# Optimization experiments

Measured on AMD Instinct MI355X. Metric: run time of the kernel, lower is better.

The kernel has to match this reference:

```python
import jax, jax.numpy as jnp
import numpy as np

N, E, B, EP = 100000, 1600000, 512, 200000
NIN, NEMB, HID, NL = 64, 64, 72, 3
EPS = 1e-5


def setup_inputs() -> dict:
    key = jax.random.key(0)
    ks = jax.random.split(key, 20)
    inp = {
        'x': jax.random.normal(ks[0], (N, NIN), jnp.float32),
        'emb': jax.random.normal(ks[1], (N, NEMB), jnp.float32),
        'assign': jax.random.uniform(ks[2], (N, B), jnp.float32),
        'edge_index': jax.random.randint(ks[3], (2, E), 0, N, jnp.int64),
        'pedge_index': jax.random.randint(ks[4], (2, EP), 0, B, jnp.int64),
        # params (xavier-ish scale)
        'node_w': jax.random.normal(ks[5], (NIN, HID), jnp.float32) / np.sqrt(NIN),
        'node_b': jnp.zeros((HID,), jnp.float32),
        'emb_w': jax.random.normal(ks[6], (NEMB, HID), jnp.float32) / np.sqrt(NEMB),
        'emb_b': jnp.zeros((HID,), jnp.float32),
        'conv_winit': jax.random.normal(ks[7], (NL, HID, HID), jnp.float32) / np.sqrt(HID),
        'conv_wroot': jax.random.normal(ks[8], (NL, HID, HID), jnp.float32) / np.sqrt(HID),
        'conv_bias': jnp.zeros((NL, HID), jnp.float32),
        'bn_gamma': jnp.ones((NL, HID), jnp.float32),
        'bn_beta': jnp.zeros((NL, HID), jnp.float32),
        'mlp_w1': jax.random.normal(ks[9], (12 * HID, HID), jnp.float32) / np.sqrt(12 * HID),
        'mlp_b1': jnp.zeros((HID,), jnp.float32),
        'mlp_w2': jax.random.normal(ks[10], (HID, 1), jnp.float32) / np.sqrt(HID),
        'mlp_b2': jnp.zeros((1,), jnp.float32),
    }
    return inp


def _forward(x, emb, assign, node_w, node_b, emb_w, emb_b, conv_winit,
             conv_wroot, conv_bias, bn_gamma, bn_beta, mlp_w1, mlp_b1,
             mlp_w2, mlp_b2, edge_index, pedge_index):
    n = x.shape[0]
    nb = assign.shape[1]
    row, col = edge_index[0], edge_index[1]
    # gcn_norm without self-loops (ARMAConv): D^{-1/2} A D^{-1/2}
    deg = jax.ops.segment_sum(jnp.ones((row.shape[0],), x.dtype), col, num_segments=n)
    dis = jnp.where(deg > 0, jax.lax.rsqrt(jnp.maximum(deg, 1.0)) * jnp.where(deg > 0, 1.0, 0.0), 0.0)
    dis = jnp.where(deg > 0, deg ** -0.5, 0.0)
    norm = dis[row] * dis[col]

    h = jax.nn.relu(x @ node_w + node_b)  # [N, HID]
    for l in range(NL):
        # ARMAConv K=1, T=1: relu(A_hat (h Wi) + h Wr + b)
        m = norm[:, None] * (h @ conv_winit[l])[row]        # [E, HID]
        agg = jax.ops.segment_sum(m, col, num_segments=n)   # [N, HID]
        h = jax.nn.relu(agg + h @ conv_wroot[l] + conv_bias[l])
        # F.relu applied again in forward (idempotent), then BatchNorm (training stats)
        mu = h.mean(0)
        var = ((h - mu) ** 2).mean(0)
        h = (h - mu) * jax.lax.rsqrt(var + EPS) * bn_gamma[l] + bn_beta[l]

    e = jax.nn.relu(emb @ emb_w + emb_b)
    z = jnp.concatenate([h, e], axis=-1)  # [N, 2*HID]

    batch = jnp.argmax(assign, axis=-1)
    cnt = jax.ops.segment_sum(jnp.ones((n,), z.dtype), batch, num_segments=nb)
    p1 = jax.ops.segment_sum(z, batch, num_segments=nb)
    p2 = jax.ops.segment_max(z, batch, num_segments=nb)
    p3 = p1 / jnp.maximum(cnt, 1.0)[:, None]
    xp = jnp.concatenate([p1, p2, p3], axis=-1)  # [B, 6*HID]

    pair = jnp.concatenate([xp[pedge_index[0]], xp[pedge_index[1]]], axis=1)  # [EP, 12*HID]
    out = jnp.tanh(pair @ mlp_w1 + mlp_b1) @ mlp_w2 + mlp_b2
    return out


def reference(x, emb, assign, edge_index, pedge_index, node_w, node_b, emb_w,
              emb_b, conv_winit, conv_wroot, conv_bias, bn_gamma, bn_beta,
              mlp_w1, mlp_b1, mlp_w2, mlp_b2):
    return _forward(x, emb, assign, node_w, node_b, emb_w, emb_b, conv_winit,
                    conv_wroot, conv_bias, bn_gamma, bn_beta, mlp_w1, mlp_b1,
                    mlp_w2, mlp_b2, edge_index, pedge_index)
```

## Files before the change

kernel.cpp:

```cpp
#include <hip/hip_runtime.h>
#include <hip/hip_bf16.h>

#define HID 72
#define EPSV 1e-5f
#define CAP 64
#define DP 76
#define GF 384
#define GA 2048

__device__ __forceinline__ float tanh_fast(float x) {
    float cx = fminf(fmaxf(x, -15.f), 15.f);
    float e = __expf(2.f * cx);
    return __fdividef(e - 1.f, e + 1.f);
}
__device__ __forceinline__ void fma4(float4& a, float w, const float4 v) {
    a.x += w * v.x; a.y += w * v.y; a.z += w * v.z; a.w += w * v.w;
}
__device__ __forceinline__ float inv_sqrt_deg(int d) {
    return (d > 0) ? rsqrtf((float)d) : 0.f;
}

__global__ __launch_bounds__(256) void k_d1(const float* __restrict__ x, const float* __restrict__ node_w,
                                            const float* __restrict__ node_b, float* __restrict__ t_buf,
                                            int* __restrict__ deg, float* __restrict__ stats,
                                            int* __restrict__ bcnt, int N, int B, int GD) {
    __shared__ float ws[HID][DP];
    int tid = threadIdx.x;
    int bid = blockIdx.x;
    if (bid >= GD) {
        int j = (bid - GD) * 256 + tid;
        if (j < N) deg[j] = 0;
        if (j < 3 * 2 * HID) stats[j] = 0.f;
        if (j < B) bcnt[j] = 0;
        return;
    }
    int n0 = bid * 128;
    for (int i = tid; i < 64 * HID; i += 256) {
        int k = i / HID, f = i % HID;
        ws[f][k] = node_w[i];
    }
    __syncthreads();
    int tn = tid & 31;
    int tf = (tid >> 5) * 9;
    float acc[4][9];
    #pragma unroll
    for (int j = 0; j < 9; j++) {
        float b = node_b[tf + j];
        acc[0][j] = b; acc[1][j] = b; acc[2][j] = b; acc[3][j] = b;
    }
    int g0 = n0 + tn;
    const float4* xp0 = (const float4*)(x + (size_t)(g0      < N ? g0      : N - 1) * 64);
    const float4* xp1 = (const float4*)(x + (size_t)(g0 + 32 < N ? g0 + 32 : N - 1) * 64);
    const float4* xp2 = (const float4*)(x + (size_t)(g0 + 64 < N ? g0 + 64 : N - 1) * 64);
    const float4* xp3 = (const float4*)(x + (size_t)(g0 + 96 < N ? g0 + 96 : N - 1) * 64);
    #pragma unroll 2
    for (int k4 = 0; k4 < 16; k4++) {
        float4 h0 = xp0[k4];
        float4 h1 = xp1[k4];
        float4 h2 = xp2[k4];
        float4 h3 = xp3[k4];
        int k = k4 * 4;
        #pragma unroll
        for (int j = 0; j < 9; j++) {
            float4 w = *(const float4*)&ws[tf + j][k];
            acc[0][j] += h0.x * w.x + h0.y * w.y + h0.z * w.z + h0.w * w.w;
            acc[1][j] += h1.x * w.x + h1.y * w.y + h1.z * w.z + h1.w * w.w;
            acc[2][j] += h2.x * w.x + h2.y * w.y + h2.z * w.z + h2.w * w.w;
            acc[3][j] += h3.x * w.x + h3.y * w.y + h3.z * w.z + h3.w * w.w;
        }
    }
    #pragma unroll
    for (int i = 0; i < 4; i++) {
        int gn = n0 + tn + 32 * i;
        if (gn >= N) continue;
        float* dst = t_buf + (size_t)gn * HID + tf;
        #pragma unroll
        for (int j = 0; j < 9; j++) dst[j] = fmaxf(acc[i][j], 0.f);
    }
}

__global__ __launch_bounds__(256) void k_front2(const int* __restrict__ row, const int* __restrict__ col,
                                                int* __restrict__ deg, int* __restrict__ csr_r, int E,
                                                const float* __restrict__ wi0, const float* __restrict__ wr0,
                                                const float* __restrict__ cb0, float* __restrict__ t_buf,
                                                float* __restrict__ hw,
                                                const float* __restrict__ emb, const float* __restrict__ emb_w,
                                                const float* __restrict__ emb_b, float* __restrict__ e_buf,
                                                const float* __restrict__ assign, int* __restrict__ batchv,
                                                int* __restrict__ bcnt, int N, int B, int GDE, int GC) {
    __shared__ float ws2[2 * HID][DP];
    int tid = threadIdx.x;
    int bid = blockIdx.x;

    if (bid < GF) {
        int stride = GF * 256 * 8;
        for (int base = (bid * 256 + tid) * 8; base < E; base += stride) {
            #pragma unroll
            for (int h = 0; h < 2; h++) {
                int eb = base + h * 4;
                if (eb + 3 < E) {
                    int4 cc = *(const int4*)(col + eb);
                    int4 rr = *(const int4*)(row + eb);
                    int p0 = atomicAdd(&deg[cc.x], 1);
                    int p1 = atomicAdd(&deg[cc.y], 1);
                    int p2 = atomicAdd(&deg[cc.z], 1);
                    int p3 = atomicAdd(&deg[cc.w], 1);
                    if (p0 < CAP) csr_r[(size_t)cc.x * CAP + p0] = rr.x;
                    if (p1 < CAP) csr_r[(size_t)cc.y * CAP + p1] = rr.y;
                    if (p2 < CAP) csr_r[(size_t)cc.z * CAP + p2] = rr.z;
                    if (p3 < CAP) csr_r[(size_t)cc.w * CAP + p3] = rr.w;
                } else if (eb < E) {
                    int lim = (eb + 4 < E) ? eb + 4 : E;
                    for (int e = eb; e < lim; e++) {
                        int c = col[e];
                        int pos = atomicAdd(&deg[c], 1);
                        if (pos < CAP) csr_r[(size_t)c * CAP + pos] = row[e];
                    }
                }
            }
        }
        return;
    }
    bid -= GF;
    if (bid < GC) {
        int n0 = bid * 64;
        for (int i = tid; i < HID * 2 * HID; i += 256) {
            int k = i / (2 * HID), f = i % (2 * HID);
            ws2[f][k] = (f < HID) ? wi0[k * HID + f] : wr0[k * HID + (f - HID)];
        }
        __syncthreads();
        int tn = tid & 15;
        int tf = (tid >> 4) * 9;
        float acc[4][9];
        #pragma unroll
        for (int j = 0; j < 9; j++) {
            float b = (tf >= HID) ? cb0[tf - HID + j] : 0.f;
            acc[0][j] = b; acc[1][j] = b; acc[2][j] = b; acc[3][j] = b;
        }
        int g0 = n0 + tn;
        const float* r0 = t_buf + (size_t)(g0      < N ? g0      : N - 1) * HID;
        const float* r1 = t_buf + (size_t)(g0 + 16 < N ? g0 + 16 : N - 1) * HID;
        const float* r2 = t_buf + (size_t)(g0 + 32 < N ? g0 + 32 : N - 1) * HID;
        const float* r3 = t_buf + (size_t)(g0 + 48 < N ? g0 + 48 : N - 1) * HID;
        #pragma unroll 2
        for (int k4 = 0; k4 < HID / 4; k4++) {
            int k = k4 * 4;
            float4 h0 = *(const float4*)(r0 + k);
            float4 h1 = *(const float4*)(r1 + k);
            float4 h2 = *(const float4*)(r2 + k);
            float4 h3 = *(const float4*)(r3 + k);
            #pragma unroll
            for (int j = 0; j < 9; j++) {
                float4 w = *(const float4*)&ws2[tf + j][k];
                acc[0][j] += h0.x * w.x + h0.y * w.y + h0.z * w.z + h0.w * w.w;
                acc[1][j] += h1.x * w.x + h1.y * w.y + h1.z * w.z + h1.w * w.w;
                acc[2][j] += h2.x * w.x + h2.y * w.y + h2.z * w.z + h2.w * w.w;
                acc[3][j] += h3.x * w.x + h3.y * w.y + h3.z * w.z + h3.w * w.w;
            }
        }
        __syncthreads();
        #pragma unroll
        for (int i = 0; i < 4; i++) {
            int gn = n0 + tn + 16 * i;
            if (gn >= N) continue;
            float* dst = (tf < HID) ? (hw + (size_t)gn * HID + tf) : (t_buf + (size_t)gn * HID + (tf - HID));
            #pragma unroll
            for (int j = 0; j < 9; j++) dst[j] = acc[i][j];
        }
        return;
    }
    bid -= GC;
    if (bid < GDE) {
        int n0 = bid * 128;
        for (int i = tid; i < 64 * HID; i += 256) {
            int k = i / HID, f = i % HID;
            ws2[f][k] = emb_w[i];
        }
        __syncthreads();
        int tn = tid & 31;
        int tf = (tid >> 5) * 9;
        float acc[4][9];
        #pragma unroll
        for (int j = 0; j < 9; j++) {
            float b = emb_b[tf + j];
            acc[0][j] = b; acc[1][j] = b; acc[2][j] = b; acc[3][j] = b;
        }
        int g0 = n0 + tn;
        const float4* xp0 = (const float4*)(emb + (size_t)(g0      < N ? g0      : N - 1) * 64);
        const float4* xp1 = (const float4*)(emb + (size_t)(g0 + 32 < N ? g0 + 32 : N - 1) * 64);
        const float4* xp2 = (const float4*)(emb + (size_t)(g0 + 64 < N ? g0 + 64 : N - 1) * 64);
        const float4* xp3 = (const float4*)(emb + (size_t)(g0 + 96 < N ? g0 + 96 : N - 1) * 64);
        #pragma unroll 2
        for (int k4 = 0; k4 < 16; k4++) {
            float4 h0 = xp0[k4];
            float4 h1 = xp1[k4];
            float4 h2 = xp2[k4];
            float4 h3 = xp3[k4];
            int k = k4 * 4;
            #pragma unroll
            for (int j = 0; j < 9; j++) {
                float4 w = *(const float4*)&ws2[tf + j][k];
                acc[0][j] += h0.x * w.x + h0.y * w.y + h0.z * w.z + h0.w * w.w;
                acc[1][j] += h1.x * w.x + h1.y * w.y + h1.z * w.z + h1.w * w.w;
                acc[2][j] += h2.x * w.x + h2.y * w.y + h2.z * w.z + h2.w * w.w;
                acc[3][j] += h3.x * w.x + h3.y * w.y + h3.z * w.z + h3.w * w.w;
            }
        }
        #pragma unroll
        for (int i = 0; i < 4; i++) {
            int gn = n0 + tn + 32 * i;
            if (gn >= N) continue;
            float* dst = e_buf + (size_t)gn * HID + tf;
            #pragma unroll
            for (int j = 0; j < 9; j++) dst[j] = fmaxf(acc[i][j], 0.f);
        }
        return;
    }
    bid -= GDE;
    int wib = tid >> 6;
    int lane = tid & 63;
    int nq = B / 4;
    for (int n = bid * 4 + wib; n < N; n += GA * 4) {
        const float4* rp4 = (const float4*)(assign + (size_t)n * B);
        float best = -INFINITY;
        int bidx = 0x7fffffff;
        for (int q = lane; q < nq; q += 64) {
            float4 v = rp4[q];
            int j = q * 4;
            if (v.x > best) { best = v.x; bidx = j; }
            if (v.y > best) { best = v.y; bidx = j + 1; }
            if (v.z > best) { best = v.z; bidx = j + 2; }
            if (v.w > best) { best = v.w; bidx = j + 3; }
        }
        #pragma unroll
        for (int off = 32; off > 0; off >>= 1) {
            float ov = __shfl_down(best, off);
            int oi = __shfl_down(bidx, off);
            if (ov > best || (ov == best && oi < bidx)) { best = ov; bidx = oi; }
        }
        if (lane == 0) {
            batchv[n] = bidx;
            atomicAdd(&bcnt[bidx], 1);
        }
    }
}

__global__ __launch_bounds__(256) void k_gather9(const float* __restrict__ hw, const int* __restrict__ deg,
                                                 const int* __restrict__ csr_r, float* t, int N,
                                                 int scanB, const int* __restrict__ bcnt,
                                                 int* __restrict__ boffs, int* __restrict__ bcur) {
    if (scanB && blockIdx.x == gridDim.x - 1) {
        int lane = threadIdx.x;
        if (lane < 64) {
            int c[8];
            int tot = 0;
            int base = lane * 8;
            #pragma unroll
            for (int j = 0; j < 8; j++) {
                int idx = base + j;
                c[j] = (idx < scanB) ? bcnt[idx] : 0;
                tot += c[j];
            }
            int v = tot;
            #pragma unroll
            for (int off = 1; off < 64; off <<= 1) {
                int u = __shfl_up(v, off);
                if (lane >= off) v += u;
            }
            int run = v - tot;
            #pragma unroll
            for (int j = 0; j < 8; j++) {
                int idx = base + j;
                if (idx < scanB) {
                    boffs[idx] = run;
                    bcur[idx] = run;
                    run += c[j];
                }
            }
        }
        return;
    }
    int tid = blockIdx.x * blockDim.x + threadIdx.x;
    int n = tid / 9;
    int s = tid - n * 9;
    if (n >= N) return;
    float4* trow = (float4*)(t + (size_t)n * HID) + s * 2;
    float4 a0 = trow[0], a1 = trow[1];
    int dn = deg[n];
    int d = (dn > CAP) ? CAP : dn;
    float disc = inv_sqrt_deg(dn);
    const int* crow = csr_r + (size_t)n * CAP;
    const float4* hb = (const float4*)hw + s * 2;
    for (int j0 = 0; j0 < d; j0 += 4) {
        int4 rr = *(const int4*)(crow + j0);
        int rem = d - j0;
        {
            float w = disc * inv_sqrt_deg(deg[rr.x]);
            const float4* hp = hb + (size_t)rr.x * 18;
            fma4(a0, w, hp[0]); fma4(a1, w, hp[1]);
        }
        if (rem > 1) {
            float w = disc * inv_sqrt_deg(deg[rr.y]);
            const float4* hp = hb + (size_t)rr.y * 18;
            fma4(a0, w, hp[0]); fma4(a1, w, hp[1]);
        }
        if (rem > 2) {
            float w = disc * inv_sqrt_deg(deg[rr.z]);
            const float4* hp = hb + (size_t)rr.z * 18;
            fma4(a0, w, hp[0]); fma4(a1, w, hp[1]);
        }
        if (rem > 3) {
            float w = disc * inv_sqrt_deg(deg[rr.w]);
            const float4* hp = hb + (size_t)rr.w * 18;
            fma4(a0, w, hp[0]); fma4(a1, w, hp[1]);
        }
    }
    trow[0] = make_float4(fmaxf(a0.x, 0.f), fmaxf(a0.y, 0.f), fmaxf(a0.z, 0.f), fmaxf(a0.w, 0.f));
    trow[1] = make_float4(fmaxf(a1.x, 0.f), fmaxf(a1.y, 0.f), fmaxf(a1.z, 0.f), fmaxf(a1.w, 0.f));
}

#define CP 76
__global__ __launch_bounds__(256) void k_conv_t(const float* t, const float* __restrict__ stats,
                                                const float* __restrict__ gamma, const float* __restrict__ beta,
                                                const float* __restrict__ wi, const float* __restrict__ wr,
                                                const float* __restrict__ cb, float* __restrict__ hw,
                                                float* agg, int N, float invN, int gcBlocks,
                                                const int* __restrict__ batchv, int* __restrict__ bcur,
                                                int* __restrict__ nlist) {
    __shared__ float hs[64][CP];
    __shared__ float ws[2 * HID][CP];
    int tid = threadIdx.x;
    if ((int)blockIdx.x >= gcBlocks) {
        int n = ((int)blockIdx.x - gcBlocks) * 256 + tid;
        if (n < N) {
            int b = batchv[n];
            int pos = atomicAdd(&bcur[b], 1);
            nlist[pos] = n;
        }
        return;
    }
    int n0 = blockIdx.x * 64;
    for (int i = tid; i < HID * 2 * HID; i += 256) {
        int k = i / (2 * HID), f = i % (2 * HID);
        ws[f][k] = (f < HID) ? wi[k * HID + f] : wr[k * HID + (f - HID)];
    }
    for (int i = tid; i < 64 * HID; i += 256) {
        int n = i / HID, f = i % HID;
        int gn = n0 + n;
        float v = (gn < N) ? t[(size_t)gn * HID + f] : 0.f;
        float mu = stats[f] * invN;
        float var = stats[HID + f] * invN - mu * mu;
        v = (v - mu) * rsqrtf(var + EPSV) * gamma[f] + beta[f];
        hs[n][f] = v;
    }
    __syncthreads();
    int tn = tid & 15;
    int tf = (tid >> 4) * 9;
    float acc[4][9];
    #pragma unroll
    for (int j = 0; j < 9; j++) {
        float b = (tf >= HID) ? cb[tf - HID + j] : 0.f;
        acc[0][j] = b; acc[1][j] = b; acc[2][j] = b; acc[3][j] = b;
    }
    #pragma unroll 2
    for (int k4 = 0; k4 < HID / 4; k4++) {
        int k = k4 * 4;
        float4 h0 = *(const float4*)&hs[tn][k];
        float4 h1 = *(const float4*)&hs[tn + 16][k];
        float4 h2 = *(const float4*)&hs[tn + 32][k];
        float4 h3 = *(const float4*)&hs[tn + 48][k];
        #pragma unroll
        for (int j = 0; j < 9; j++) {
            float4 w = *(const float4*)&ws[tf + j][k];
            acc[0][j] += h0.x * w.x + h0.y * w.y + h0.z * w.z + h0.w * w.w;
            acc[1][j] += h1.x * w.x + h1.y * w.y + h1.z * w.z + h1.w * w.w;
            acc[2][j] += h2.x * w.x + h2.y * w.y + h2.z * w.z + h2.w * w.w;
            acc[3][j] += h3.x * w.x + h3.y * w.y + h3.z * w.z + h3.w * w.w;
        }
    }
    #pragma unroll
    for (int i = 0; i < 4; i++) {
        int gn = n0 + tn + 16 * i;
        if (gn >= N) continue;
        float* dst = (tf < HID) ? (hw + (size_t)gn * HID + tf) : (agg + (size_t)gn * HID + (tf - HID));
        #pragma unroll
        for (int j = 0; j < 9; j++) dst[j] = acc[i][j];
    }
}

__global__ __launch_bounds__(256) void k_stats(const float* __restrict__ t, float* __restrict__ st, int total4) {
    __shared__ float s1[HID], s2[HID];
    int tx = threadIdx.x;
    if (tx < HID) s1[tx] = 0.f;
    else if (tx < 2 * HID) s2[tx - HID] = 0.f;
    __syncthreads();
    int stride = gridDim.x * blockDim.x;
    int i0 = blockIdx.x * blockDim.x + tx;
    int f0 = (i0 * 4) % HID;
    float a0 = 0, a1 = 0, a2 = 0, a3 = 0, q0 = 0, q1 = 0, q2 = 0, q3 = 0;
    const float4* tp = (const float4*)t;
    for (int i = i0; i < total4; i += stride) {
        float4 v = tp[i];
        a0 += v.x; q0 += v.x * v.x;
        a1 += v.y; q1 += v.y * v.y;
        a2 += v.z; q2 += v.z * v.z;
        a3 += v.w; q3 += v.w * v.w;
    }
    atomicAdd(&s1[f0 + 0], a0); atomicAdd(&s2[f0 + 0], q0);
    atomicAdd(&s1[f0 + 1], a1); atomicAdd(&s2[f0 + 1], q1);
    atomicAdd(&s1[f0 + 2], a2); atomicAdd(&s2[f0 + 2], q2);
    atomicAdd(&s1[f0 + 3], a3); atomicAdd(&s2[f0 + 3], q3);
    __syncthreads();
    if (tx < HID) {
        atomicAdd(&st[tx], s1[tx]);
        atomicAdd(&st[HID + tx], s2[tx]);
    }
}

__global__ __launch_bounds__(576) void k_poolB(const float* __restrict__ t2, const float* __restrict__ ebuf,
                                               const float* __restrict__ stats2, const float* __restrict__ g2,
                                               const float* __restrict__ bt2, const int* __restrict__ boffs,
                                               const int* __restrict__ bcnt, const int* __restrict__ nlist,
                                               float* __restrict__ xp, float invN) {
    __shared__ float ls[4][2 * HID], lm[4][2 * HID];
    int b = blockIdx.x;
    int tid = threadIdx.x;
    int f = tid % (2 * HID);
    int ch = tid / (2 * HID);
    bool isH = f < HID;
    float a = 1.f, sh = 0.f;
    const float* src;
    if (isH) {
        float s1v = stats2[f], s2v = stats2[HID + f];
        float mu = s1v * invN;
        float var = s2v * invN - mu * mu;
        float inv = rsqrtf(var + EPSV);
        a = inv * g2[f];
        sh = bt2[f] - mu * a;
        src = t2 + f;
    } else {
        src = ebuf + (f - HID);
    }
    int s = boffs[b];
    int c = bcnt[b];
    int e = s + c;
    float sum = 0.f, mx = -INFINITY;
    for (int i = s + ch; i < e; i += 4) {
        float v = src[(size_t)nlist[i] * HID] * a + sh;
        sum += v;
        mx = fmaxf(mx, v);
    }
    ls[ch][f] = sum;
    lm[ch][f] = mx;
    __syncthreads();
    if (ch == 0) {
        float stot = ls[0][f] + ls[1][f] + ls[2][f] + ls[3][f];
        float mtot = fmaxf(fmaxf(lm[0][f], lm[1][f]), fmaxf(lm[2][f], lm[3][f]));
        float* xr = xp + (size_t)b * (6 * HID);
        xr[f] = stot;
        xr[2 * HID + f] = mtot;
        xr[4 * HID + f] = stot / fmaxf((float)c, 1.f);
    }
}

__global__ __launch_bounds__(192) void k_uv(const float* __restrict__ xp, const float* __restrict__ w1,
                                            const float* __restrict__ b1, float* __restrict__ U,
                                            float* __restrict__ V) {
    int b = blockIdx.x;
    int t = threadIdx.x;
    if (t >= 2 * HID) return;
    int half = t / HID;
    int f = t % HID;
    const float* xr = xp + (size_t)b * (6 * HID);
    const float* wb = w1 + (size_t)half * (6 * HID) * HID + f;
    float acc = (half == 0) ? b1[f] : 0.f;
    #pragma unroll 4
    for (int k = 0; k < 6 * HID; k++) acc += xr[k] * wb[(size_t)k * HID];
    if (half == 0) U[(size_t)b * HID + f] = acc;
    else           V[(size_t)b * HID + f] = acc;
}

__global__ __launch_bounds__(256) void k_edge(const int* __restrict__ pe, const float* __restrict__ U,
                                              const float* __restrict__ V, const float* __restrict__ w2,
                                              const float* __restrict__ b2, float* __restrict__ out, int EP) {
    int ep = blockIdx.x * blockDim.x + threadIdx.x;
    if (ep >= EP) return;
    int a = pe[ep];
    int b = pe[EP + ep];
    const float4* up = (const float4*)(U + (size_t)a * HID);
    const float4* vp = (const float4*)(V + (size_t)b * HID);
    float s = 0.f;
    #pragma unroll
    for (int q = 0; q < HID / 4; q++) {
        float4 u = up[q];
        float4 v = vp[q];
        s += tanh_fast(u.x + v.x) * w2[q * 4 + 0];
        s += tanh_fast(u.y + v.y) * w2[q * 4 + 1];
        s += tanh_fast(u.z + v.z) * w2[q * 4 + 2];
        s += tanh_fast(u.w + v.w) * w2[q * 4 + 3];
    }
    out[ep] = s + b2[0];
}

extern "C" void kernel_launch(void* const* d_in, const int* in_sizes, int n_in,
                              void* d_out, int out_size, void* d_ws, size_t ws_size,
                              hipStream_t stream) {
    const float* x       = (const float*)d_in[0];
    const float* emb     = (const float*)d_in[1];
    const float* assign  = (const float*)d_in[2];
    const int*   ei      = (const int*)d_in[3];
    const int*   pe      = (const int*)d_in[4];
    const float* node_w  = (const float*)d_in[5];
    const float* node_b  = (const float*)d_in[6];
    const float* emb_w   = (const float*)d_in[7];
    const float* emb_b   = (const float*)d_in[8];
    const float* conv_wi = (const float*)d_in[9];
    const float* conv_wr = (const float*)d_in[10];
    const float* conv_b  = (const float*)d_in[11];
    const float* bn_g    = (const float*)d_in[12];
    const float* bn_b    = (const float*)d_in[13];
    const float* w1      = (const float*)d_in[14];
    const float* b1      = (const float*)d_in[15];
    const float* w2      = (const float*)d_in[16];
    const float* b2      = (const float*)d_in[17];

    int N = in_sizes[0] / 64;
    int B = in_sizes[2] / N;
    int E = in_sizes[3] / 2;
    int EP = in_sizes[4] / 2;
    float invN = 1.0f / (float)N;

    char* wp = (char*)d_ws;
    auto alloc = [&](size_t nbytes) -> void* {
        void* p = (void*)wp;
        wp += (nbytes + 255) & ~(size_t)255;
        return p;
    };
    float* t_buf  = (float*)alloc((size_t)N * HID * 4);
    float* hw     = (float*)alloc((size_t)N * HID * 4);
    float* e_buf  = (float*)alloc((size_t)N * HID * 4);
    int*   csr_r  = (int*)alloc((size_t)N * CAP * 4);
    int*   deg    = (int*)alloc((size_t)N * 4);
    int*   batchv = (int*)alloc((size_t)N * 4);
    int*   nlist  = (int*)alloc((size_t)N * 4);
    float* stats  = (float*)alloc((size_t)3 * 2 * HID * 4);
    int*   bcnt   = (int*)alloc((size_t)B * 4);
    int*   boffs  = (int*)alloc((size_t)B * 4);
    int*   bcur   = (int*)alloc((size_t)B * 4);
    float* xp     = (float*)alloc((size_t)B * 6 * HID * 4);
    float* Ub     = (float*)alloc((size_t)B * HID * 4);
    float* Vb     = (float*)alloc((size_t)B * HID * 4);

    const int* row = ei;
    const int* col = ei + E;

    int GD = (N + 127) / 128;
    int GC = (N + 63) / 64;
    int GZ = (N + 255) / 256;
    int GG = (9 * N + 255) / 256;

    k_d1<<<GD + GZ, 256, 0, stream>>>(x, node_w, node_b, t_buf, deg, stats, bcnt, N, B, GD);

    k_front2<<<GF + GC + GD + GA, 256, 0, stream>>>(row, col, deg, csr_r, E,
                                                    conv_wi, conv_wr, conv_b, t_buf, hw,
                                                    emb, emb_w, emb_b, e_buf,
                                                    assign, batchv, bcnt, N, B, GD, GC);

    k_gather9<<<GG + 1, 256, 0, stream>>>(hw, deg, csr_r, t_buf, N, B, bcnt, boffs, bcur);
    k_stats<<<288, 256, 0, stream>>>(t_buf, stats, N * HID / 4);

    k_conv_t<<<GC + GZ, 256, 0, stream>>>(t_buf, stats, bn_g, bn_b,
                                          conv_wi + (size_t)HID * HID, conv_wr + (size_t)HID * HID,
                                          conv_b + HID, hw, t_buf, N, invN, GC, batchv, bcur, nlist);
    k_gather9<<<GG, 256, 0, stream>>>(hw, deg, csr_r, t_buf, N, 0, nullptr, nullptr, nullptr);
    k_stats<<<288, 256, 0, stream>>>(t_buf, stats + 2 * HID, N * HID / 4);

    k_conv_t<<<GC, 256, 0, stream>>>(t_buf, stats + 2 * HID, bn_g + HID, bn_b + HID,
                                     conv_wi + (size_t)2 * HID * HID, conv_wr + (size_t)2 * HID * HID,
                                     conv_b + 2 * HID, hw, t_buf, N, invN, GC, nullptr, nullptr, nullptr);
    k_gather9<<<GG, 256, 0, stream>>>(hw, deg, csr_r, t_buf, N, 0, nullptr, nullptr, nullptr);
    k_stats<<<288, 256, 0, stream>>>(t_buf, stats + 4 * HID, N * HID / 4);

    k_poolB<<<B, 576, 0, stream>>>(t_buf, e_buf, stats + 4 * HID,
                                   bn_g + 2 * HID, bn_b + 2 * HID,
                                   boffs, bcnt, nlist, xp, invN);
    k_uv<<<B, 192, 0, stream>>>(xp, w1, b1, Ub, Vb);
    k_edge<<<(EP + 255) / 256, 256, 0, stream>>>(pe, Ub, Vb, w2, b2, (float*)d_out, EP);
}
```

Baseline: 1.227 ms.

## Fuse BN stats into gather, prescale hw by source degree, rebalance front kernels

Removes the three k_stats passes by accumulating per-feature sum and sum of squares inside the gather kernel, using block-level shared atomics and then 32 shadow copies in global memory to spread contention. conv_t now multiplies hw by the source node's inverse sqrt degree, so later gathers add neighbour rows without looking up each neighbour's degree. The emb projection moves into k_d1, and the layer-0 conv is split into separate Wi and Wr blocks, with the root term written to a new t2 buffer instead of in place. The costs are an extra N×HID buffer, per-element shared atomics in the gather, and reduced-order float sums for the statistics.

Result: slower. 1.316 ms (+7.2%).

```diff
diff --git a/kernel.cpp b/kernel.cpp
--- a/kernel.cpp
+++ b/kernel.cpp
@@ -5,7 +5,8 @@
 #define EPSV 1e-5f
 #define CAP 64
 #define DP 76
-#define GF 384
+#define NSH 32
+#define GF 256
 #define GA 2048
 
 __device__ __forceinline__ float tanh_fast(float x) {
@@ -16,28 +17,37 @@
 __device__ __forceinline__ void fma4(float4& a, float w, const float4 v) {
     a.x += w * v.x; a.y += w * v.y; a.z += w * v.z; a.w += w * v.w;
 }
+__device__ __forceinline__ void add4(float4& a, const float4 v) {
+    a.x += v.x; a.y += v.y; a.z += v.z; a.w += v.w;
+}
 __device__ __forceinline__ float inv_sqrt_deg(int d) {
     return (d > 0) ? rsqrtf((float)d) : 0.f;
 }
 
 __global__ __launch_bounds__(256) void k_d1(const float* __restrict__ x, const float* __restrict__ node_w,
-                                            const float* __restrict__ node_b, float* __restrict__ t_buf,
-                                            int* __restrict__ deg, float* __restrict__ stats,
+                                            const float* __restrict__ node_b,
+                                            const float* __restrict__ emb, const float* __restrict__ emb_w,
+                                            const float* __restrict__ emb_b,
+                                            float* __restrict__ t_buf, float* __restrict__ e_buf,
+                                            int* __restrict__ deg, float* __restrict__ shadows,
                                             int* __restrict__ bcnt, int N, int B, int GD) {
     __shared__ float ws[HID][DP];
     int tid = threadIdx.x;
     int bid = blockIdx.x;
-    if (bid >= GD) {
-        int j = (bid - GD) * 256 + tid;
+    if (bid >= 2 * GD) {
+        int j = (bid - 2 * GD) * 256 + tid;
         if (j < N) deg[j] = 0;
-        if (j < 3 * 2 * HID) stats[j] = 0.f;
+        if (j < 3 * NSH * 2 * HID) shadows[j] = 0.f;
         if (j < B) bcnt[j] = 0;
         return;
     }
+    const float* xin; const float* W; const float* bias; float* out;
+    if (bid < GD) { xin = x;   W = node_w; bias = node_b; out = t_buf; }
+    else          { xin = emb; W = emb_w;  bias = emb_b;  out = e_buf; bid -= GD; }
     int n0 = bid * 128;
     for (int i = tid; i < 64 * HID; i += 256) {
         int k = i / HID, f = i % HID;
-        ws[f][k] = node_w[i];
+        ws[f][k] = W[i];
     }
     __syncthreads();
     int tn = tid & 31;
@@ -45,14 +55,14 @@
     float acc[4][9];
     #pragma unroll
     for (int j = 0; j < 9; j++) {
-        float b = node_b[tf + j];
+        float b = bias[tf + j];
         acc[0][j] = b; acc[1][j] = b; acc[2][j] = b; acc[3][j] = b;
     }
     int g0 = n0 + tn;
-    const float4* xp0 = (const float4*)(x + (size_t)(g0      < N ? g0      : N - 1) * 64);
-    const float4* xp1 = (const float4*)(x + (size_t)(g0 + 32 < N ? g0 + 32 : N - 1) * 64);
-    const float4* xp2 = (const float4*)(x + (size_t)(g0 + 64 < N ? g0 + 64 : N - 1) * 64);
-    const float4* xp3 = (const float4*)(x + (size_t)(g0 + 96 < N ? g0 + 96 : N - 1) * 64);
+    const float4* xp0 = (const float4*)(xin + (size_t)(g0      < N ? g0      : N - 1) * 64);
+    const float4* xp1 = (const float4*)(xin + (size_t)(g0 + 32 < N ? g0 + 32 : N - 1) * 64);
+    const float4* xp2 = (const float4*)(xin + (size_t)(g0 + 64 < N ? g0 + 64 : N - 1) * 64);
+    const float4* xp3 = (const float4*)(xin + (size_t)(g0 + 96 < N ? g0 + 96 : N - 1) * 64);
     #pragma unroll 2
     for (int k4 = 0; k4 < 16; k4++) {
         float4 h0 = xp0[k4];
@@ -73,7 +83,7 @@
     for (int i = 0; i < 4; i++) {
         int gn = n0 + tn + 32 * i;
         if (gn >= N) continue;
-        float* dst = t_buf + (size_t)gn * HID + tf;
+        float* dst = out + (size_t)gn * HID + tf;
         #pragma unroll
         for (int j = 0; j < 9; j++) dst[j] = fmaxf(acc[i][j], 0.f);
     }
@@ -81,14 +91,13 @@
 
 __global__ __launch_bounds__(256) void k_front2(const int* __restrict__ row, const int* __restrict__ col,
                                                 int* __restrict__ deg, int* __restrict__ csr_r, int E,
+                                                const float* __restrict__ t_buf,
                                                 const float* __restrict__ wi0, const float* __restrict__ wr0,
-                                                const float* __restrict__ cb0, float* __restrict__ t_buf,
-                                                float* __restrict__ hw,
-                                                const float* __restrict__ emb, const float* __restrict__ emb_w,
-                                                const float* __restrict__ emb_b, float* __restrict__ e_buf,
+                                                const float* __restrict__ cb0,
+                                                float* __restrict__ hw, float* __restrict__ t2,
                                                 const float* __restrict__ assign, int* __restrict__ batchv,
-                                                int* __restrict__ bcnt, int N, int B, int GDE, int GC) {
-    __shared__ float ws2[2 * HID][DP];
+                                                int* __restrict__ bcnt, int N, int B, int GC) {
+    __shared__ float ws[HID][DP];
     int tid = threadIdx.x;
     int bid = blockIdx.x;
 
@@ -122,26 +131,29 @@
         return;
     }
     bid -= GF;
-    if (bid < GC) {
-        int n0 = bid * 64;
-        for (int i = tid; i < HID * 2 * HID; i += 256) {
-            int k = i / (2 * HID), f = i % (2 * HID);
-            ws2[f][k] = (f < HID) ? wi0[k * HID + f] : wr0[k * HID + (f - HID)];
+    if (bid < 2 * GC) {
+        const float* W; const float* bias; float* out;
+        if (bid < GC) { W = wi0; bias = nullptr; out = hw; }
+        else          { W = wr0; bias = cb0;     out = t2; bid -= GC; }
+        int n0 = bid * 128;
+        for (int i = tid; i < HID * HID; i += 256) {
+            int k = i / HID, f = i % HID;
+            ws[f][k] = W[i];
         }
         __syncthreads();
-        int tn = tid & 15;
-        int tf = (tid >> 4) * 9;
+        int tn = tid & 31;
+        int tf = (tid >> 5) * 9;
         float acc[4][9];
         #pragma unroll
         for (int j = 0; j < 9; j++) {
-            float b = (tf >= HID) ? cb0[tf - HID + j] : 0.f;
+            float b = bias ? bias[tf + j] : 0.f;
             acc[0][j] = b; acc[1][j] = b; acc[2][j] = b; acc[3][j] = b;
         }
         int g0 = n0 + tn;
         const float* r0 = t_buf + (size_t)(g0      < N ? g0      : N - 1) * HID;
-        const float* r1 = t_buf + (size_t)(g0 + 16 < N ? g0 + 16 : N - 1) * HID;
-        const float* r2 = t_buf + (size_t)(g0 + 32 < N ? g0 + 32 : N - 1) * HID;
-        const float* r3 = t_buf + (size_t)(g0 + 48 < N ? g0 + 48 : N - 1) * HID;
+        const float* r1 = t_buf + (size_t)(g0 + 32 < N ? g0 + 32 : N - 1) * HID;
+        const float* r2 = t_buf + (size_t)(g0 + 64 < N ? g0 + 64 : N - 1) * HID;
+        const float* r3 = t_buf + (size_t)(g0 + 96 < N ? g0 + 96 : N - 1) * HID;
         #pragma unroll 2
         for (int k4 = 0; k4 < HID / 4; k4++) {
             int k = k4 * 4;
@@ -151,72 +163,24 @@
             float4 h3 = *(const float4*)(r3 + k);
             #pragma unroll
             for (int j = 0; j < 9; j++) {
-                float4 w = *(const float4*)&ws2[tf + j][k];
+                float4 w = *(const float4*)&ws[tf + j][k];
                 acc[0][j] += h0.x * w.x + h0.y * w.y + h0.z * w.z + h0.w * w.w;
                 acc[1][j] += h1.x * w.x + h1.y * w.y + h1.z * w.z + h1.w * w.w;
                 acc[2][j] += h2.x * w.x + h2.y * w.y + h2.z * w.z + h2.w * w.w;
                 acc[3][j] += h3.x * w.x + h3.y * w.y + h3.z * w.z + h3.w * w.w;
             }
         }
-        __syncthreads();
-        #pragma unroll
-        for (int i = 0; i < 4; i++) {
-            int gn = n0 + tn + 16 * i;
-            if (gn >= N) continue;
-            float* dst = (tf < HID) ? (hw + (size_t)gn * HID + tf) : (t_buf + (size_t)gn * HID + (tf - HID));
-            #pragma unroll
-            for (int j = 0; j < 9; j++) dst[j] = acc[i][j];
-        }
-        return;
-    }
-    bid -= GC;
-    if (bid < GDE) {
-        int n0 = bid * 128;
-        for (int i = tid; i < 64 * HID; i += 256) {
-            int k = i / HID, f = i % HID;
-            ws2[f][k] = emb_w[i];
-        }
-        __syncthreads();
-        int tn = tid & 31;
-        int tf = (tid >> 5) * 9;
-        float acc[4][9];
-        #pragma unroll
-        for (int j = 0; j < 9; j++) {
-            float b = emb_b[tf + j];
-            acc[0][j] = b; acc[1][j] = b; acc[2][j] = b; acc[3][j] = b;
-        }
-        int g0 = n0 + tn;
-        const float4* xp0 = (const float4*)(emb + (size_t)(g0      < N ? g0      : N - 1) * 64);
-        const float4* xp1 = (const float4*)(emb + (size_t)(g0 + 32 < N ? g0 + 32 : N - 1) * 64);
-        const float4* xp2 = (const float4*)(emb + (size_t)(g0 + 64 < N ? g0 + 64 : N - 1) * 64);
-        const float4* xp3 = (const float4*)(emb + (size_t)(g0 + 96 < N ? g0 + 96 : N - 1) * 64);
-        #pragma unroll 2
-        for (int k4 = 0; k4 < 16; k4++) {
-            float4 h0 = xp0[k4];
-            float4 h1 = xp1[k4];
-            float4 h2 = xp2[k4];
-            float4 h3 = xp3[k4];
-            int k = k4 * 4;
-            #pragma unroll
-            for (int j = 0; j < 9; j++) {
-                float4 w = *(const float4*)&ws2[tf + j][k];
-                acc[0][j] += h0.x * w.x + h0.y * w.y + h0.z * w.z + h0.w * w.w;
-                acc[1][j] += h1.x * w.x + h1.y * w.y + h1.z * w.z + h1.w * w.w;
-                acc[2][j] += h2.x * w.x + h2.y * w.y + h2.z * w.z + h2.w * w.w;
-                acc[3][j] += h3.x * w.x + h3.y * w.y + h3.z * w.z + h3.w * w.w;
-            }
-        }
         #pragma unroll
         for (int i = 0; i < 4; i++) {
             int gn = n0 + tn + 32 * i;
             if (gn >= N) continue;
-            float* dst = e_buf + (size_t)gn * HID + tf;
-            #pragma unroll
-            for (int j = 0; j < 9; j++) dst[j] = fmaxf(acc[i][j], 0.f);
+            float* dst = out + (size_t)gn * HID + tf;
+            #pragma unroll
+            for (int j = 0; j < 9; j++) dst[j] = acc[i][j];
         }
         return;
     }
-    bid -= GDE;
+    bid -= 2 * GC;
     int wib = tid >> 6;
     int lane = tid & 63;
     int nq = B / 4;
@@ -245,8 +209,10 @@
     }
 }
 
+template <int SCALED>
 __global__ __launch_bounds__(256) void k_gather9(const float* __restrict__ hw, const int* __restrict__ deg,
-                                                 const int* __restrict__ csr_r, float* t, int N,
+                                                 const int* __restrict__ csr_r, const float* __restrict__ t2,
+                                                 float* __restrict__ t, int N, float* __restrict__ shadow,
                                                  int scanB, const int* __restrict__ bcnt,
                                                  int* __restrict__ boffs, int* __restrict__ bcur) {
     if (scanB && blockIdx.x == gridDim.x - 1) {
@@ -280,55 +246,83 @@
         }
         return;
     }
-    int tid = blockIdx.x * blockDim.x + threadIdx.x;
+    __shared__ float s1[HID], s2[HID];
+    int tx = threadIdx.x;
+    if (tx < HID) { s1[tx] = 0.f; s2[tx] = 0.f; }
+    __syncthreads();
+    int tid = blockIdx.x * blockDim.x + tx;
     int n = tid / 9;
     int s = tid - n * 9;
-    if (n >= N) return;
-    float4* trow = (float4*)(t + (size_t)n * HID) + s * 2;
-    float4 a0 = trow[0], a1 = trow[1];
-    int dn = deg[n];
-    int d = (dn > CAP) ? CAP : dn;
-    float disc = inv_sqrt_deg(dn);
-    const int* crow = csr_r + (size_t)n * CAP;
-    const float4* hb = (const float4*)hw + s * 2;
-    for (int j0 = 0; j0 < d; j0 += 4) {
-        int4 rr = *(const int4*)(crow + j0);
-        int rem = d - j0;
-        {
-            float w = disc * inv_sqrt_deg(deg[rr.x]);
-            const float4* hp = hb + (size_t)rr.x * 18;
-            fma4(a0, w, hp[0]); fma4(a1, w, hp[1]);
-        }
-        if (rem > 1) {
-            float w = disc * inv_sqrt_deg(deg[rr.y]);
-            const float4* hp = hb + (size_t)rr.y * 18;
-            fma4(a0, w, hp[0]); fma4(a1, w, hp[1]);
-        }
-        if (rem > 2) {
-            float w = disc * inv_sqrt_deg(deg[rr.z]);
-            const float4* hp = hb + (size_t)rr.z * 18;
-            fma4(a0, w, hp[0]); fma4(a1, w, hp[1]);
-        }
-        if (rem > 3) {
-            float w = disc * inv_sqrt_deg(deg[rr.w]);
-            const float4* hp = hb + (size_t)rr.w * 18;
-            fma4(a0, w, hp[0]); fma4(a1, w, hp[1]);
-        }
-    }
-    trow[0] = make_float4(fmaxf(a0.x, 0.f), fmaxf(a0.y, 0.f), fmaxf(a0.z, 0.f), fmaxf(a0.w, 0.f));
-    trow[1] = make_float4(fmaxf(a1.x, 0.f), fmaxf(a1.y, 0.f), fmaxf(a1.z, 0.f), fmaxf(a1.w, 0.f));
+    if (n < N) {
+        const float4* t2row = (const float4*)(t2 + (size_t)n * HID) + s * 2;
+        float4 a0 = t2row[0], a1 = t2row[1];
+        float4 b0 = make_float4(0.f, 0.f, 0.f, 0.f), b1 = b0;
+        int dn = deg[n];
+        int d = (dn > CAP) ? CAP : dn;
+        float disc = inv_sqrt_deg(dn);
+        const int* crow = csr_r + (size_t)n * CAP;
+        const float4* hb = (const float4*)hw + s * 2;
+        for (int j0 = 0; j0 < d; j0 += 4) {
+            int4 rr = *(const int4*)(crow + j0);
+            int rem = d - j0;
+            {
+                const float4* hp = hb + (size_t)rr.x * 18;
+                if (SCALED) { add4(b0, hp[0]); add4(b1, hp[1]); }
+                else { float w = inv_sqrt_deg(deg[rr.x]); fma4(b0, w, hp[0]); fma4(b1, w, hp[1]); }
+            }
+            if (rem > 1) {
+                const float4* hp = hb + (size_t)rr.y * 18;
+                if (SCALED) { add4(b0, hp[0]); add4(b1, hp[1]); }
+                else { float w = inv_sqrt_deg(deg[rr.y]); fma4(b0, w, hp[0]); fma4(b1, w, hp[1]); }
+            }
+            if (rem > 2) {
+                const float4* hp = hb + (size_t)rr.z * 18;
+                if (SCALED) { add4(b0, hp[0]); add4(b1, hp[1]); }
+                else { float w = inv_sqrt_deg(deg[rr.z]); fma4(b0, w, hp[0]); fma4(b1, w, hp[1]); }
+            }
+            if (rem > 3) {
+                const float4* hp = hb + (size_t)rr.w * 18;
+                if (SCALED) { add4(b0, hp[0]); add4(b1, hp[1]); }
+                else { float w = inv_sqrt_deg(deg[rr.w]); fma4(b0, w, hp[0]); fma4(b1, w, hp[1]); }
+            }
+        }
+        fma4(a0, disc, b0);
+        fma4(a1, disc, b1);
+        a0 = make_float4(fmaxf(a0.x, 0.f), fmaxf(a0.y, 0.f), fmaxf(a0.z, 0.f), fmaxf(a0.w, 0.f));
+        a1 = make_float4(fmaxf(a1.x, 0.f), fmaxf(a1.y, 0.f), fmaxf(a1.z, 0.f), fmaxf(a1.w, 0.f));
+        float4* trow = (float4*)(t + (size_t)n * HID) + s * 2;
+        trow[0] = a0;
+        trow[1] = a1;
+        int f0 = s * 8;
+        atomicAdd(&s1[f0 + 0], a0.x); atomicAdd(&s2[f0 + 0], a0.x * a0.x);
+        atomicAdd(&s1[f0 + 1], a0.y); atomicAdd(&s2[f0 + 1], a0.y * a0.y);
+        atomicAdd(&s1[f0 + 2], a0.z); atomicAdd(&s2[f0 + 2], a0.z * a0.z);
+        atomicAdd(&s1[f0 + 3], a0.w); atomicAdd(&s2[f0 + 3], a0.w * a0.w);
+        atomicAdd(&s1[f0 + 4], a1.x); atomicAdd(&s2[f0 + 4], a1.x * a1.x);
+        atomicAdd(&s1[f0 + 5], a1.y); atomicAdd(&s2[f0 + 5], a1.y * a1.y);
+        atomicAdd(&s1[f0 + 6], a1.z); atomicAdd(&s2[f0 + 6], a1.z * a1.z);
+        atomicAdd(&s1[f0 + 7], a1.w); atomicAdd(&s2[f0 + 7], a1.w * a1.w);
+    }
+    __syncthreads();
+    if (tx < HID) {
+        float* shrow = shadow + (size_t)(blockIdx.x & (NSH - 1)) * (2 * HID);
+        atomicAdd(&shrow[tx], s1[tx]);
+        atomicAdd(&shrow[HID + tx], s2[tx]);
+    }
 }
 
 #define CP 76
-__global__ __launch_bounds__(256) void k_conv_t(const float* t, const float* __restrict__ stats,
+__global__ __launch_bounds__(256) void k_conv_t(const float* __restrict__ t, const float* __restrict__ shadow,
                                                 const float* __restrict__ gamma, const float* __restrict__ beta,
                                                 const float* __restrict__ wi, const float* __restrict__ wr,
                                                 const float* __restrict__ cb, float* __restrict__ hw,
-                                                float* agg, int N, float invN, int gcBlocks,
+                                                float* __restrict__ t2, const int* __restrict__ deg,
+                                                int N, float invN, int gcBlocks,
                                                 const int* __restrict__ batchv, int* __restrict__ bcur,
                                                 int* __restrict__ nlist) {
     __shared__ float hs[64][CP];
     __shared__ float ws[2 * HID][CP];
+    __shared__ float bns[2 * HID];
     int tid = threadIdx.x;
     if ((int)blockIdx.x >= gcBlocks) {
         int n = ((int)blockIdx.x - gcBlocks) * 256 + tid;
@@ -339,17 +333,24 @@
         }
         return;
     }
-    int n0 = blockIdx.x * 64;
+    if (tid < 2 * HID) {
+        float ssum = 0.f;
+        #pragma unroll
+        for (int c = 0; c < NSH; c++) ssum += shadow[c * 2 * HID + tid];
+        bns[tid] = ssum;
+    }
     for (int i = tid; i < HID * 2 * HID; i += 256) {
         int k = i / (2 * HID), f = i % (2 * HID);
         ws[f][k] = (f < HID) ? wi[k * HID + f] : wr[k * HID + (f - HID)];
     }
+    __syncthreads();
+    int n0 = blockIdx.x * 64;
     for (int i = tid; i < 64 * HID; i += 256) {
         int n = i / HID, f = i % HID;
         int gn = n0 + n;
         float v = (gn < N) ? t[(size_t)gn * HID + f] : 0.f;
-        float mu = stats[f] * invN;
-        float var = stats[HID + f] * invN - mu * mu;
+        float mu = bns[f] * invN;
+        float var = bns[HID + f] * invN - mu * mu;
         v = (v - mu) * rsqrtf(var + EPSV) * gamma[f] + beta[f];
         hs[n][f] = v;
     }
@@ -382,43 +383,21 @@
     for (int i = 0; i < 4; i++) {
         int gn = n0 + tn + 16 * i;
         if (gn >= N) continue;
-        float* dst = (tf < HID) ? (hw + (size_t)gn * HID + tf) : (agg + (size_t)gn * HID + (tf - HID));
-        #pragma unroll
-        for (int j = 0; j < 9; j++) dst[j] = acc[i][j];
-    }
-}
-
-__global__ __launch_bounds__(256) void k_stats(const float* __restrict__ t, float* __restrict__ st, int total4) {
-    __shared__ float s1[HID], s2[HID];
-    int tx = threadIdx.x;
-    if (tx < HID) s1[tx] = 0.f;
-    else if (tx < 2 * HID) s2[tx - HID] = 0.f;
-    __syncthreads();
-    int stride = gridDim.x * blockDim.x;
-    int i0 = blockIdx.x * blockDim.x + tx;
-    int f0 = (i0 * 4) % HID;
-    float a0 = 0, a1 = 0, a2 = 0, a3 = 0, q0 = 0, q1 = 0, q2 = 0, q3 = 0;
-    const float4* tp = (const float4*)t;
-    for (int i = i0; i < total4; i += stride) {
-        float4 v = tp[i];
-        a0 += v.x; q0 += v.x * v.x;
-        a1 += v.y; q1 += v.y * v.y;
-        a2 += v.z; q2 += v.z * v.z;
-        a3 += v.w; q3 += v.w * v.w;
-    }
-    atomicAdd(&s1[f0 + 0], a0); atomicAdd(&s2[f0 + 0], q0);
-    atomicAdd(&s1[f0 + 1], a1); atomicAdd(&s2[f0 + 1], q1);
-    atomicAdd(&s1[f0 + 2], a2); atomicAdd(&s2[f0 + 2], q2);
-    atomicAdd(&s1[f0 + 3], a3); atomicAdd(&s2[f0 + 3], q3);
-    __syncthreads();
-    if (tx < HID) {
-        atomicAdd(&st[tx], s1[tx]);
-        atomicAdd(&st[HID + tx], s2[tx]);
+        if (tf < HID) {
+            float dsc = inv_sqrt_deg(deg[gn]);
+            float* dst = hw + (size_t)gn * HID + tf;
+            #pragma unroll
+            for (int j = 0; j < 9; j++) dst[j] = acc[i][j] * dsc;
+        } else {
+            float* dst = t2 + (size_t)gn * HID + (tf - HID);
+            #pragma unroll
+            for (int j = 0; j < 9; j++) dst[j] = acc[i][j];
+        }
     }
 }
 
 __global__ __launch_bounds__(576) void k_poolB(const float* __restrict__ t2, const float* __restrict__ ebuf,
-                                               const float* __restrict__ stats2, const float* __restrict__ g2,
+                                               const float* __restrict__ shadow2, const float* __restrict__ g2,
                                                const float* __restrict__ bt2, const int* __restrict__ boffs,
                                                const int* __restrict__ bcnt, const int* __restrict__ nlist,
                                                float* __restrict__ xp, float invN) {
@@ -431,7 +410,12 @@
     float a = 1.f, sh = 0.f;
     const float* src;
     if (isH) {
-        float s1v = stats2[f], s2v = stats2[HID + f];
+        float s1v = 0.f, s2v = 0.f;
+        #pragma unroll
+        for (int c = 0; c < NSH; c++) {
+            s1v += shadow2[c * 2 * HID + f];
+            s2v += shadow2[c * 2 * HID + HID + f];
+        }
         float mu = s1v * invN;
         float var = s2v * invN - mu * mu;
         float inv = rsqrtf(var + EPSV);
@@ -537,13 +521,14 @@
         return p;
     };
     float* t_buf  = (float*)alloc((size_t)N * HID * 4);
+    float* t2     = (float*)alloc((size_t)N * HID * 4);
     float* hw     = (float*)alloc((size_t)N * HID * 4);
     float* e_buf  = (float*)alloc((size_t)N * HID * 4);
     int*   csr_r  = (int*)alloc((size_t)N * CAP * 4);
     int*   deg    = (int*)alloc((size_t)N * 4);
     int*   batchv = (int*)alloc((size_t)N * 4);
     int*   nlist  = (int*)alloc((size_t)N * 4);
-    float* stats  = (float*)alloc((size_t)3 * 2 * HID * 4);
+    float* shadows= (float*)alloc((size_t)3 * NSH * 2 * HID * 4);
     int*   bcnt   = (int*)alloc((size_t)B * 4);
     int*   boffs  = (int*)alloc((size_t)B * 4);
     int*   bcur   = (int*)alloc((size_t)B * 4);
@@ -554,34 +539,37 @@
     const int* row = ei;
     const int* col = ei + E;
 
-    int GD = (N + 127) / 128;
-    int GC = (N + 63) / 64;
-    int GZ = (N + 255) / 256;
-    int GG = (9 * N + 255) / 256;
-
-    k_d1<<<GD + GZ, 256, 0, stream>>>(x, node_w, node_b, t_buf, deg, stats, bcnt, N, B, GD);
-
-    k_front2<<<GF + GC + GD + GA, 256, 0, stream>>>(row, col, deg, csr_r, E,
-                                                    conv_wi, conv_wr, conv_b, t_buf, hw,
-                                                    emb, emb_w, emb_b, e_buf,
-                                                    assign, batchv, bcnt, N, B, GD, GC);
-
-    k_gather9<<<GG + 1, 256, 0, stream>>>(hw, deg, csr_r, t_buf, N, B, bcnt, boffs, bcur);
-    k_stats<<<288, 256, 0, stream>>>(t_buf, stats, N * HID / 4);
-
-    k_conv_t<<<GC + GZ, 256, 0, stream>>>(t_buf, stats, bn_g, bn_b,
-                                          conv_wi + (size_t)HID * HID, conv_wr + (size_t)HID * HID,
-                                          conv_b + HID, hw, t_buf, N, invN, GC, batchv, bcur, nlist);
-    k_gather9<<<GG, 256, 0, stream>>>(hw, deg, csr_r, t_buf, N, 0, nullptr, nullptr, nullptr);
-    k_stats<<<288, 256, 0, stream>>>(t_buf, stats + 2 * HID, N * HID / 4);
-
-    k_conv_t<<<GC, 256, 0, stream>>>(t_buf, stats + 2 * HID, bn_g + HID, bn_b + HID,
-                                     conv_wi + (size_t)2 * HID * HID, conv_wr + (size_t)2 * HID * HID,
-                                     conv_b + 2 * HID, hw, t_buf, N, invN, GC, nullptr, nullptr, nullptr);
-    k_gather9<<<GG, 256, 0, stream>>>(hw, deg, csr_r, t_buf, N, 0, nullptr, nullptr, nullptr);
-    k_stats<<<288, 256, 0, stream>>>(t_buf, stats + 4 * HID, N * HID / 4);
-
-    k_poolB<<<B, 576, 0, stream>>>(t_buf, e_buf, stats + 4 * HID,
+    int GD   = (N + 127) / 128;
+    int GC64 = (N + 63) / 64;
+    int GZ   = (N + 255) / 256;
+    int GG   = (9 * N + 255) / 256;
+    size_t shl = (size_t)NSH * 2 * HID;
+
+    k_d1<<<2 * GD + GZ, 256, 0, stream>>>(x, node_w, node_b, emb, emb_w, emb_b,
+                                          t_buf, e_buf, deg, shadows, bcnt, N, B, GD);
+
+    k_front2<<<GF + 2 * GD + GA, 256, 0, stream>>>(row, col, deg, csr_r, E,
+                                                   t_buf, conv_wi, conv_wr, conv_b, hw, t2,
+                                                   assign, batchv, bcnt, N, B, GD);
+
+    k_gather9<0><<<GG + 1, 256, 0, stream>>>(hw, deg, csr_r, t2, t_buf, N, shadows,
+                                             B, bcnt, boffs, bcur);
+
+    k_conv_t<<<GC64 + GZ, 256, 0, stream>>>(t_buf, shadows, bn_g, bn_b,
+                                            conv_wi + (size_t)HID * HID, conv_wr + (size_t)HID * HID,
+                                            conv_b + HID, hw, t2, deg, N, invN, GC64,
+                                            batchv, bcur, nlist);
+    k_gather9<1><<<GG, 256, 0, stream>>>(hw, deg, csr_r, t2, t_buf, N, shadows + shl,
+                                         0, nullptr, nullptr, nullptr);
+
+    k_conv_t<<<GC64, 256, 0, stream>>>(t_buf, shadows + shl, bn_g + HID, bn_b + HID,
+                                       conv_wi + (size_t)2 * HID * HID, conv_wr + (size_t)2 * HID * HID,
+                                       conv_b + 2 * HID, hw, t2, deg, N, invN, GC64,
+                                       nullptr, nullptr, nullptr);
+    k_gather9<1><<<GG, 256, 0, stream>>>(hw, deg, csr_r, t2, t_buf, N, shadows + 2 * shl,
+                                         0, nullptr, nullptr, nullptr);
+
+    k_poolB<<<B, 576, 0, stream>>>(t_buf, e_buf, shadows + 2 * shl,
                                    bn_g + 2 * HID, bn_b + 2 * HID,
                                    boffs, bcnt, nlist, xp, invN);
     k_uv<<<B, 192, 0, stream>>>(xp, w1, b1, Ub, Vb);
```
